# Kernel tuning notes

Measured on AMD Instinct MI355X. Metric: run time of the kernel, lower is better.

## Reference

```python
import jax, jax.numpy as jnp
import numpy as np

B, F, NB, E = 32768, 64, 64, 32


def setup_inputs() -> dict:
    key = jax.random.key(0)
    k1, k2, k3, k4 = jax.random.split(key, 4)
    x = jax.random.normal(k1, (B, F), dtype=jnp.float32)
    # per-feature sorted bin edges (as produced by PLE.adapt quantiles)
    bins = jnp.sort(jax.random.uniform(k2, (F, NB), dtype=jnp.float32,
                                       minval=-2.0, maxval=2.0), axis=1)
    W = jax.random.normal(k3, (F, NB, E), dtype=jnp.float32) / np.sqrt(NB)
    b = jax.random.normal(k4, (F, E), dtype=jnp.float32)
    return {"x": x, "bins": bins, "W": W, "b": b}


def reference(x, bins, W, b):
    # x: [B,F], bins: [F,NB] sorted edges, W: [F,NB,E], b: [F,E]
    nb = bins.shape[1]
    lo = bins  # bins[j] == lookup_table[i-1] for bin i=j+1
    # lookup_table.get(i, -1): last bin has no upper edge -> defaults to -1.0
    hi = jnp.concatenate(
        [bins[:, 1:], jnp.full((bins.shape[0], 1), -1.0, bins.dtype)], axis=1)
    j = jnp.arange(nb)
    xe = x[:, :, None]                                  # [B,F,1]
    left = (xe < lo[None]) & (j > 0)                    # [B,F,NB]
    right = (xe >= hi[None]) & (j < nb - 1)             # [B,F,NB]
    v = (xe - lo[None]) / (hi - lo)[None]               # interpolation value
    # enc = 0 where left, 1 where neither, v where exactly one of left/right
    enc = jnp.where(left != right, v, jnp.where(left, 0.0, 1.0))  # [B,F,NB]
    # per-feature linear + ReLU, then features stacked along dim 1
    emb = jax.nn.relu(jnp.einsum('bfn,fne->bfe', enc, W) + b[None])  # [B,F,E]
    return emb
```

## Files before the change

### kernel.cpp

```cpp
#include <hip/hip_runtime.h>


#define FDIM 64
#define NB   64
#define EDIM 32
#define FSL  8
#define NRPB 256
#define ITERS (NRPB / 32)
#define SWSTR 34

typedef __attribute__((ext_vector_type(4))) float f32x4;

static __device__ __forceinline__ unsigned bf16rne(float f) {
    unsigned u = __float_as_uint(f);
    return (u + 0x7FFFu + ((u >> 16) & 1u)) >> 16;
}

__global__ __launch_bounds__(256) void nemb_fused(
    const float* __restrict__ x, const float* __restrict__ bins,
    const float* __restrict__ W, const float* __restrict__ bias,
    float* __restrict__ out)
{
    __shared__ unsigned short sW16[FSL * NB * SWSTR];
    __shared__ float sBins[FSL * 65];
    __shared__ float sP[FSL * EDIM];
    __shared__ float sR[FSL * EDIM];

    const int t     = threadIdx.x;
    const int slice = blockIdx.x & 7;
    const int chunk = blockIdx.x >> 3;
    const int f0    = slice * FSL;

    const int w  = t >> 6;
    const int l  = t & 63;
    const int rs = l >> 3;
    const int fs = l & 7;
    const int ft = l >> 3;
    const int e0 = (l & 7) * 4;

    const long r00 = (long)chunk * NRPB;

    float xpre[ITERS];
    #pragma unroll
    for (int it = 0; it < ITERS; ++it)
        xpre[it] = x[(r00 + it * 32 + w * 8 + rs) * FDIM + f0 + fs];

    float bias_v = bias[(f0 + (t >> 5)) * EDIM + (t & 31)];

    const float* Wg = W + (size_t)f0 * NB * EDIM;
    unsigned* sWd = reinterpret_cast<unsigned*>(sW16);
    #pragma unroll
    for (int i = 0; i < 16; ++i) {
        int qi = i * 256 + t;
        f32x4 v = reinterpret_cast<const f32x4*>(Wg)[qi];
        int gi = qi * 4;
        int fl = gi >> 11;
        int n  = (gi >> 5) & 63;
        int ee = gi & 31;
        unsigned u0 = bf16rne(v.x) | (bf16rne(v.y) << 16);
        unsigned u1 = bf16rne(v.z) | (bf16rne(v.w) << 16);
        int d0 = 17 * (fl * 64 + n) + (ee >> 1);
        sWd[d0]     = u0;
        sWd[d0 + 1] = u1;
    }
    if (t < 128) {
        f32x4 v = reinterpret_cast<const f32x4*>(bins + (size_t)f0 * NB)[t];
        int gi = t * 4;
        int fl = gi >> 6, n = gi & 63;
        float* d = &sBins[fl * 65 + n];
        d[0] = v.x; d[1] = v.y; d[2] = v.z; d[3] = v.w;
    }
    if (t < FSL) sBins[t * 65 + 64] = -1.0f;
    __syncthreads();

    {
        const int fl = t >> 5;
        const int e  = t & 31;
        float p = 0.0f, q = 0.0f;
        #pragma unroll
        for (int n = 0; n < NB; ++n) {
            float lo = sBins[fl * 65 + n];
            float hi = sBins[fl * 65 + n + 1];
            float gv = __builtin_amdgcn_rcpf(hi - lo);
            float wv = __uint_as_float((unsigned)sW16[(fl * 64 + n) * SWSTR + e] << 16);
            p = fmaf(gv, wv, p);
            q = fmaf(lo * gv, wv, q);
        }
        sP[fl * EDIM + e] = p;
        sR[fl * EDIM + e] = bias_v - q;
    }
    __syncthreads();

    const f32x4 Pv = *reinterpret_cast<const f32x4*>(&sP[ft * EDIM + e0]);
    const f32x4 Rv = *reinterpret_cast<const f32x4*>(&sR[ft * EDIM + e0]);

    const float* bl = &sBins[fs * 65];
    const int bp_base = (l >> 3) * 4;

    #pragma unroll
    for (int it = 0; it < ITERS; ++it) {
        const long rb = r00 + it * 32 + w * 8;
        float xv = xpre[it];

        int k = 0;
        k += (bl[ 8] <= xv) ? 8 : 0;
        k += (bl[16] <= xv) ? 8 : 0;
        k += (bl[24] <= xv) ? 8 : 0;
        k += (bl[32] <= xv) ? 8 : 0;
        k += (bl[40] <= xv) ? 8 : 0;
        k += (bl[48] <= xv) ? 8 : 0;
        k += (bl[56] <= xv) ? 8 : 0;
        {
            const float* b2 = bl + k;
            int inner = 0;
            inner += (b2[1] <= xv) ? 1 : 0;
            inner += (b2[2] <= xv) ? 1 : 0;
            inner += (b2[3] <= xv) ? 1 : 0;
            inner += (b2[4] <= xv) ? 1 : 0;
            inner += (b2[5] <= xv) ? 1 : 0;
            inner += (b2[6] <= xv) ? 1 : 0;
            inner += (b2[7] <= xv) ? 1 : 0;
            k += inner;
        }
        float lo = bl[k];
        float hi = bl[k + 1];
        float cv = (hi - xv) * __builtin_amdgcn_rcpf(hi - lo);

        #pragma unroll
        for (int r = 0; r < 8; ++r) {
            const int a = bp_base + r * 32;
            float xr = __uint_as_float((unsigned)
                __builtin_amdgcn_ds_bpermute(a, (int)__float_as_uint(xv)));
            float cr = __uint_as_float((unsigned)
                __builtin_amdgcn_ds_bpermute(a, (int)__float_as_uint(cv)));
            int   kr = __builtin_amdgcn_ds_bpermute(a, k);

            int d0 = 17 * (ft * 64 + kr) + ((l & 7) << 1);
            unsigned u0 = sWd[d0];
            unsigned u1 = sWd[d0 + 1];
            f32x4 Wv;
            Wv.x = __uint_as_float(u0 << 16);
            Wv.y = __uint_as_float(u0 & 0xFFFF0000u);
            Wv.z = __uint_as_float(u1 << 16);
            Wv.w = __uint_as_float(u1 & 0xFFFF0000u);

            f32x4 o;
            o.x = fmaxf(fmaf(cr, Wv.x, fmaf(xr, Pv.x, Rv.x)), 0.0f);
            o.y = fmaxf(fmaf(cr, Wv.y, fmaf(xr, Pv.y, Rv.y)), 0.0f);
            o.z = fmaxf(fmaf(cr, Wv.z, fmaf(xr, Pv.z, Rv.z)), 0.0f);
            o.w = fmaxf(fmaf(cr, Wv.w, fmaf(xr, Pv.w, Rv.w)), 0.0f);
            *reinterpret_cast<f32x4*>(
                out + (rb + r) * (FDIM * EDIM) + (f0 + ft) * EDIM + e0) = o;
        }
    }
}

extern "C" void kernel_launch(void* const* d_in, const int* in_sizes, int n_in,
                              void* d_out, int out_size, void* d_ws, size_t ws_size,
                              hipStream_t stream) {
    const float* x    = (const float*)d_in[0];
    const float* bins = (const float*)d_in[1];
    const float* W    = (const float*)d_in[2];
    const float* bias = (const float*)d_in[3];
    float* out = (float*)d_out;

    const int B = in_sizes[0] / FDIM;
    const int nchunks = B / NRPB;

    nemb_fused<<<nchunks * 8, 256, 0, stream>>>(x, bins, W, bias, out);
}
```

Measured before the change: 52.05 us.

## Overlap W staging with bin search and pack bin index into coefficient

Loads bins first, then runs the per-row bin search while the first half of W is in flight, so global W load latency overlaps with the search. W is staged in two halves of 8 vectors to cap register pressure. The bin index is packed into the low 6 mantissa bits of the interpolation coefficient, which removes one ds_bpermute per output row. This adds an extra barrier and a small precision loss in the coefficient.

```diff
diff --git a/kernel.cpp b/kernel.cpp
--- a/kernel.cpp
+++ b/kernel.cpp
@@ -40,29 +40,6 @@
 
     const long r00 = (long)chunk * NRPB;
 
-    float xpre[ITERS];
-    #pragma unroll
-    for (int it = 0; it < ITERS; ++it)
-        xpre[it] = x[(r00 + it * 32 + w * 8 + rs) * FDIM + f0 + fs];
-
-    float bias_v = bias[(f0 + (t >> 5)) * EDIM + (t & 31)];
-
-    const float* Wg = W + (size_t)f0 * NB * EDIM;
-    unsigned* sWd = reinterpret_cast<unsigned*>(sW16);
-    #pragma unroll
-    for (int i = 0; i < 16; ++i) {
-        int qi = i * 256 + t;
-        f32x4 v = reinterpret_cast<const f32x4*>(Wg)[qi];
-        int gi = qi * 4;
-        int fl = gi >> 11;
-        int n  = (gi >> 5) & 63;
-        int ee = gi & 31;
-        unsigned u0 = bf16rne(v.x) | (bf16rne(v.y) << 16);
-        unsigned u1 = bf16rne(v.z) | (bf16rne(v.w) << 16);
-        int d0 = 17 * (fl * 64 + n) + (ee >> 1);
-        sWd[d0]     = u0;
-        sWd[d0 + 1] = u1;
-    }
     if (t < 128) {
         f32x4 v = reinterpret_cast<const f32x4*>(bins + (size_t)f0 * NB)[t];
         int gi = t * 4;
@@ -71,6 +48,72 @@
         d[0] = v.x; d[1] = v.y; d[2] = v.z; d[3] = v.w;
     }
     if (t < FSL) sBins[t * 65 + 64] = -1.0f;
+    __syncthreads();
+
+    float xpre[ITERS];
+    #pragma unroll
+    for (int it = 0; it < ITERS; ++it)
+        xpre[it] = x[(r00 + it * 32 + w * 8 + rs) * FDIM + f0 + fs];
+    float bias_v = bias[(f0 + (t >> 5)) * EDIM + (t & 31)];
+
+    const float* Wg = W + (size_t)f0 * NB * EDIM;
+    unsigned* sWd = reinterpret_cast<unsigned*>(sW16);
+
+    f32x4 vstg[8];
+    #pragma unroll
+    for (int i = 0; i < 8; ++i)
+        vstg[i] = reinterpret_cast<const f32x4*>(Wg)[i * 256 + t];
+
+    const float* bl = &sBins[fs * 65];
+    unsigned pk[ITERS];
+    #pragma unroll
+    for (int it = 0; it < ITERS; ++it) {
+        float xv = xpre[it];
+        int k = 0;
+        k += (bl[ 8] <= xv) ? 8 : 0;
+        k += (bl[16] <= xv) ? 8 : 0;
+        k += (bl[24] <= xv) ? 8 : 0;
+        k += (bl[32] <= xv) ? 8 : 0;
+        k += (bl[40] <= xv) ? 8 : 0;
+        k += (bl[48] <= xv) ? 8 : 0;
+        k += (bl[56] <= xv) ? 8 : 0;
+        const float* b2 = bl + k;
+        int inner = 0;
+        inner += (b2[1] <= xv) ? 1 : 0;
+        inner += (b2[2] <= xv) ? 1 : 0;
+        inner += (b2[3] <= xv) ? 1 : 0;
+        inner += (b2[4] <= xv) ? 1 : 0;
+        inner += (b2[5] <= xv) ? 1 : 0;
+        inner += (b2[6] <= xv) ? 1 : 0;
+        inner += (b2[7] <= xv) ? 1 : 0;
+        k += inner;
+        float lo = bl[k];
+        float hi = bl[k + 1];
+        float cv = (hi - xv) * __builtin_amdgcn_rcpf(hi - lo);
+        pk[it] = (__float_as_uint(cv) & ~63u) | (unsigned)k;
+    }
+
+    #pragma unroll
+    for (int i = 0; i < 8; ++i) {
+        int gi = (i * 256 + t) * 4;
+        int fl = gi >> 11, n = (gi >> 5) & 63, ee = gi & 31;
+        unsigned u0 = bf16rne(vstg[i].x) | (bf16rne(vstg[i].y) << 16);
+        unsigned u1 = bf16rne(vstg[i].z) | (bf16rne(vstg[i].w) << 16);
+        int d0 = 17 * (fl * 64 + n) + (ee >> 1);
+        sWd[d0] = u0; sWd[d0 + 1] = u1;
+    }
+    #pragma unroll
+    for (int i = 8; i < 16; ++i)
+        vstg[i - 8] = reinterpret_cast<const f32x4*>(Wg)[i * 256 + t];
+    #pragma unroll
+    for (int i = 8; i < 16; ++i) {
+        int gi = (i * 256 + t) * 4;
+        int fl = gi >> 11, n = (gi >> 5) & 63, ee = gi & 31;
+        unsigned u0 = bf16rne(vstg[i - 8].x) | (bf16rne(vstg[i - 8].y) << 16);
+        unsigned u1 = bf16rne(vstg[i - 8].z) | (bf16rne(vstg[i - 8].w) << 16);
+        int d0 = 17 * (fl * 64 + n) + (ee >> 1);
+        sWd[d0] = u0; sWd[d0 + 1] = u1;
+    }
     __syncthreads();
 
     {
@@ -93,47 +136,22 @@
 
     const f32x4 Pv = *reinterpret_cast<const f32x4*>(&sP[ft * EDIM + e0]);
     const f32x4 Rv = *reinterpret_cast<const f32x4*>(&sR[ft * EDIM + e0]);
-
-    const float* bl = &sBins[fs * 65];
     const int bp_base = (l >> 3) * 4;
 
     #pragma unroll
     for (int it = 0; it < ITERS; ++it) {
         const long rb = r00 + it * 32 + w * 8;
-        float xv = xpre[it];
-
-        int k = 0;
-        k += (bl[ 8] <= xv) ? 8 : 0;
-        k += (bl[16] <= xv) ? 8 : 0;
-        k += (bl[24] <= xv) ? 8 : 0;
-        k += (bl[32] <= xv) ? 8 : 0;
-        k += (bl[40] <= xv) ? 8 : 0;
-        k += (bl[48] <= xv) ? 8 : 0;
-        k += (bl[56] <= xv) ? 8 : 0;
-        {
-            const float* b2 = bl + k;
-            int inner = 0;
-            inner += (b2[1] <= xv) ? 1 : 0;
-            inner += (b2[2] <= xv) ? 1 : 0;
-            inner += (b2[3] <= xv) ? 1 : 0;
-            inner += (b2[4] <= xv) ? 1 : 0;
-            inner += (b2[5] <= xv) ? 1 : 0;
-            inner += (b2[6] <= xv) ? 1 : 0;
-            inner += (b2[7] <= xv) ? 1 : 0;
-            k += inner;
-        }
-        float lo = bl[k];
-        float hi = bl[k + 1];
-        float cv = (hi - xv) * __builtin_amdgcn_rcpf(hi - lo);
+        const float    xv  = xpre[it];
+        const unsigned pkv = pk[it];
 
         #pragma unroll
         for (int r = 0; r < 8; ++r) {
             const int a = bp_base + r * 32;
             float xr = __uint_as_float((unsigned)
                 __builtin_amdgcn_ds_bpermute(a, (int)__float_as_uint(xv)));
-            float cr = __uint_as_float((unsigned)
-                __builtin_amdgcn_ds_bpermute(a, (int)__float_as_uint(cv)));
-            int   kr = __builtin_amdgcn_ds_bpermute(a, k);
+            unsigned pr = (unsigned)__builtin_amdgcn_ds_bpermute(a, (int)pkv);
+            int   kr = (int)(pr & 63u);
+            float cr = __uint_as_float(pr & ~63u);
 
             int d0 = 17 * (ft * 64 + kr) + ((l & 7) << 1);
             unsigned u0 = sWd[d0];
```

Result: no change. 51.89 us, median of 2 (-0.3%).
